# Kernel optimization log

Measured on AMD Instinct MI355X. Metric: run time of the kernel, lower is better.

The kernel has to match this reference:

```python
import jax, jax.numpy as jnp
import numpy as np

# module hyper-params (init_kwargs); shift_sz=1 => 1x1 patches == pixels, flag == mask
SHIFT_SZ = 1
STRIDE = 1
MASK_THRED = 1
TRIPLE_WEIGHT = 1.0   # only rescales gradients in the original custom backward; forward output unchanged
FUSE = True
FUSE_K = 3            # contextual-attention fuse kernel size (identity 3x3)


def _fuse_scores(score, H, W):
    # score: [B, L, L] (query loc, key loc). Contextual-attention 'fuse':
    # smooth the score map with an identity kernel along both spatial unfoldings.
    B, L, _ = score.shape
    eye = jnp.eye(FUSE_K, dtype=score.dtype).reshape(1, 1, FUSE_K, FUSE_K)

    def conv(x):
        return jax.lax.conv_general_dilated(
            x, eye, window_strides=(1, 1), padding='SAME',
            dimension_numbers=('NCHW', 'OIHW', 'NCHW'))

    s = conv(score[:, None])                                            # [B,1,L,L]
    s = s.reshape(B, H, W, H, W).transpose(0, 2, 1, 4, 3).reshape(B, 1, L, L)
    s = conv(s)
    s = s.reshape(B, W, H, W, H).transpose(0, 2, 1, 4, 3).reshape(B, L, L)
    return s


def reference(x, mask):
    # x: [B, 2c, H, W]; first c channels = former (decoder feat), last c = latter (encoder feat)
    B, C2, H, W = x.shape
    c = C2 // 2
    L = H * W
    former = x[:, :c]
    latter = x[:, c:]

    # flag: True = inside hole. With shift_sz=1, stride=1, mask_thred=1 the patch flag is the mask itself.
    flag = mask.reshape(L) > 0.5                                        # [L]

    lat = latter.reshape(B, c, L)
    # normalize context (key) patches to unit L2 norm -> cosine-style correlation
    key = lat / jnp.maximum(jnp.linalg.norm(lat, axis=1, keepdims=True), 1e-4)
    score = jnp.einsum('bcl,bck->blk', lat, key)                        # [B, L(query), L(key)]
    if FUSE:
        score = _fuse_scores(score, H, W)

    # only attend to context patches OUTSIDE the hole
    score = jnp.where(flag[None, None, :], -jnp.inf, score)
    attn = jax.nn.softmax(score, axis=-1)                               # [B, L, L]

    # soft shift: attention-weighted gather of former (decoder) features from context pixels
    shift = jnp.einsum('blk,bck->bcl', attn, former.reshape(B, c, L))   # [B, c, L]
    # the shifted feature only fills hole locations; zero elsewhere
    shift = shift * flag[None, None, :].astype(x.dtype)
    shift = shift.reshape(B, c, H, W)

    return jnp.concatenate([former, latter, shift], axis=1)             # [B, 3c, H, W]


def setup_inputs():
    key = jax.random.key(0)
    k1, k2 = jax.random.split(key)
    B, c, H, W = 2, 64, 64, 64
    x = jax.random.normal(k1, (B, 2 * c, H, W), dtype=jnp.float32)
    mask = (jax.random.uniform(k2, (1, 1, H, W)) > 0.75).astype(jnp.float32)
    return {"x": x, "mask": mask}
```

## Files before the change

kernel.cpp:

```cpp
#include <hip/hip_runtime.h>
#include <math.h>


#define L 4096

typedef unsigned int   u32;
typedef unsigned short u16;
typedef short  short8 __attribute__((ext_vector_type(8)));
typedef float  f32x16 __attribute__((ext_vector_type(16)));

#define MFMA32(a, b, c) __builtin_amdgcn_mfma_f32_32x32x16_bf16((a), (b), (c), 0, 0, 0)

__device__ __forceinline__ u16 f2bf(float f) {
    u32 u = __float_as_uint(f);
    u32 r = (u + 0x7FFFu + ((u >> 16) & 1u)) >> 16;
    return (u16)r;
}

__device__ __forceinline__ void lds_async16(void* lds, const void* g) {
    __builtin_amdgcn_global_load_lds((const __attribute__((address_space(1))) u32*)g,
                                     (__attribute__((address_space(3))) u32*)lds, 16, 0, 0);
}

#define OFF_LATB  0u
#define OFF_FORB  1048576u
#define OFF_GARR  2097152u
#define GARR_BB   1575936u
#define OFF_FBITS 5249024u
#define OFF_ROWS  5249536u
#define OFF_CNT   5265920u
#define OFF_PART  5266432u
#define OFF_KNB   5266432u

__global__ void k_pre1(const float4* __restrict__ x4, float4* __restrict__ out4,
                       const float* __restrict__ x, const float* __restrict__ mask,
                       u16* __restrict__ latb, u16* __restrict__ knb, u16* __restrict__ forb,
                       int* __restrict__ rows, int* __restrict__ cnt, u32* __restrict__ fbits)
{
    const int blk = blockIdx.x, t = threadIdx.x;
    if (blk < 1537) {
        int i = blk * 256 + t;
        if (i < 262144) {
            int b = i >> 17, j = i & 131071;
            out4[b * 196608 + j] = x4[b * 131072 + j];
        } else if (i < 393216) {
            int z = i - 262144; int b = z >> 16, j = z & 65535;
            out4[b * 196608 + 131072 + j] = make_float4(0.f, 0.f, 0.f, 0.f);
        }
    } else if (blk < 1569) {
        int tid = (blk - 1537) * 256 + t;
        int b = tid >> 12, l = tid & 4095;
        const float* xb = x + (size_t)b * 524288;
        float v[64]; float ss = 0.f;
        #pragma unroll
        for (int c = 0; c < 64; ++c) { v[c] = xb[(64 + c) * 4096 + l]; ss += v[c] * v[c]; }
        float inv = 1.f / fmaxf(sqrtf(ss), 1e-4f);
        u16* lr = latb + (size_t)(b * 4096 + l) * 64;
        u16* kr = knb  + (size_t)(b * 4096 + l) * 64;
        #pragma unroll
        for (int c8 = 0; c8 < 8; ++c8) {
            u32 wl[4], wk[4];
            #pragma unroll
            for (int i = 0; i < 4; ++i) {
                float a = v[c8 * 8 + 2 * i], bb2 = v[c8 * 8 + 2 * i + 1];
                wl[i] = (u32)f2bf(a) | ((u32)f2bf(bb2) << 16);
                wk[i] = (u32)f2bf(a * inv) | ((u32)f2bf(bb2 * inv) << 16);
            }
            uint4 pl = make_uint4(wl[0], wl[1], wl[2], wl[3]);
            uint4 pk = make_uint4(wk[0], wk[1], wk[2], wk[3]);
            *(uint4*)(lr + c8 * 8) = pl;
            *(uint4*)(kr + c8 * 8) = pk;
        }
        u16* fr = forb + (size_t)(b * 4096 + l) * 64;
        #pragma unroll
        for (int c8 = 0; c8 < 8; ++c8) {
            u32 wf[4];
            #pragma unroll
            for (int i = 0; i < 4; ++i) {
                float a = xb[(c8 * 8 + 2 * i) * 4096 + l];
                float bb2 = xb[(c8 * 8 + 2 * i + 1) * 4096 + l];
                wf[i] = (u32)f2bf(a) | ((u32)f2bf(bb2) << 16);
            }
            uint4 pf = make_uint4(wf[0], wf[1], wf[2], wf[3]);
            *(uint4*)(fr + c8 * 8) = pf;
        }
    } else {
        __shared__ int lcnt;
        __shared__ u32 lb[128];
        if (t == 0) lcnt = 0;
        if (t < 128) lb[t] = 0u;
        __syncthreads();
        for (int i = t; i < L; i += 256) {
            if (mask[i] > 0.5f) {
                int p = atomicAdd(&lcnt, 1); rows[p] = i;
                int kp = ((i & 63) << 6) | (i >> 6);
                atomicOr(&lb[kp >> 5], 1u << (kp & 31));
            }
        }
        __syncthreads();
        if (t < 128) fbits[t] = lb[t];
        if (t == 0) cnt[0] = lcnt;
    }
}

__global__ void k_garr(const u16* __restrict__ knb, char* __restrict__ garr)
{
    int tid = blockIdx.x * 256 + threadIdx.x;
    if (tid >= 2 * 4104 * 3) return;
    int b = tid / 12312; int rem = tid - b * 12312;
    int sg = rem / 3, aa = rem - 3 * (rem / 3);
    int mp = sg - 1;
    char* dst = garr + (size_t)b * GARR_BB + (size_t)sg * 384;
    int key = (sg & 7) << 4;
    const u16* src = nullptr;
    if (mp >= 0 && mp < L) {
        int q = (((mp & 63) << 6) | (mp >> 6)) + aa - 1;
        if (q >= 0 && q < L) src = knb + (size_t)b * 262144 + (size_t)q * 64;
    }
    #pragma unroll
    for (int c8 = 0; c8 < 8; ++c8) {
        uint4 v = src ? *(const uint4*)(src + c8 * 8) : make_uint4(0, 0, 0, 0);
        *(uint4*)(dst + ((aa * 128 + c8 * 16) ^ key)) = v;
    }
}

__global__ __launch_bounds__(256, 2)
void k_flash(const u16* __restrict__ latb, const u16* __restrict__ forb,
             const char* __restrict__ garr, const u32* __restrict__ fbits,
             const int* __restrict__ rows, const int* __restrict__ cnt,
             char* __restrict__ part)
{
    __shared__ __align__(16) char smem[80000];
    char* slab = smem;
    u16*  F_s  = (u16*)(smem + 52224);
    u16*  p_s  = (u16*)(smem + 69632);
    int*  rl_s = (int*)(smem + 79872);

    const int t = threadIdx.x;
    const int rt = blockIdx.x, ks = blockIdx.y, b = blockIdx.z;
    const int count = cnt[0];
    const int base = rt * 32;
    if (base >= count) return;
    const int nact = min(32, count - base);
    if (t < 32) rl_s[t] = rows[base + min(t, nact - 1)];
    __syncthreads();

    const int l = t & 63, w = t >> 6;
    const int li = l & 31, hi = l >> 5;
    const size_t boff = (size_t)b * 262144;

    const u16* zp = (const u16*)garr;
    int gl = rl_s[li];
    int tl0 = ((gl & 63) << 6) | (gl >> 6);
    const u16* rp[9];
    #pragma unroll
    for (int tap = 0; tap < 9; ++tap) {
        int bb = tap / 3, aa = tap - 3 * (tap / 3);
        int mp = tl0 + bb - 1;
        const u16* p = zp;
        if (mp >= 0 && mp < L) {
            int q = (((mp & 63) << 6) | (mp >> 6)) + aa - 1;
            if (q >= 0 && q < L) p = latb + boff + (size_t)q * 64;
        }
        rp[tap] = p;
    }
    short8 bu[36];
    #pragma unroll
    for (int q = 0; q < 36; ++q) {
        int tap = q >> 2, Ksi = q & 3;
        bu[q] = *(const short8*)(rp[tap] + Ksi * 16 + hi * 8);
    }

    float mrun = -INFINITY, srun = 0.f;
    f32x16 acc0, acc1;
    #pragma unroll
    for (int r = 0; r < 16; ++r) { acc0[r] = 0.f; acc1[r] = 0.f; }

    const int kp0 = ks * 512;
    const char* gb = garr + (size_t)b * GARR_BB;

    for (int kt = 0; kt < 4; ++kt) {
        const int k0p = kp0 + kt * 128;
        __syncthreads();

        const char* gw = gb + (size_t)k0p * 384;
        #pragma unroll
        for (int i = 0; i < 13; ++i) {
            int idx = w + 4 * i;
            if (idx < 51)
                lds_async16(slab + idx * 1024, gw + idx * 1024 + l * 16);
        }

        {
            int kpA = k0p + 2 * l, kpB = kpA + 1;
            int kA = ((kpA & 63) << 6) | (kpA >> 6);
            int kB = ((kpB & 63) << 6) | (kpB >> 6);
            const u32* pa = (const u32*)(forb + boff + (size_t)kA * 64 + w * 16);
            const u32* pc = (const u32*)(forb + boff + (size_t)kB * 64 + w * 16);
            uint4 A0 = *(const uint4*)pa, A1 = *(const uint4*)(pa + 4);
            uint4 B0 = *(const uint4*)pc, B1 = *(const uint4*)(pc + 4);
            u32 av[8] = {A0.x, A0.y, A0.z, A0.w, A1.x, A1.y, A1.z, A1.w};
            u32 bv[8] = {B0.x, B0.y, B0.z, B0.w, B1.x, B1.y, B1.z, B1.w};
            #pragma unroll
            for (int i2 = 0; i2 < 8; ++i2) {
                u32 w0 = (av[i2] & 0xffffu) | (bv[i2] << 16);
                u32 w1 = (av[i2] >> 16) | (bv[i2] & 0xffff0000u);
                *(u32*)((char*)F_s + (w * 16 + 2 * i2) * 272 + l * 4) = w0;
                *(u32*)((char*)F_s + (w * 16 + 2 * i2 + 1) * 272 + l * 4) = w1;
            }
        }
        asm volatile("s_waitcnt vmcnt(0)" ::: "memory");
        __syncthreads();

        f32x16 sc;
        #pragma unroll
        for (int r = 0; r < 16; ++r) sc[r] = 0.f;
        const int slot_base = w * 32 + li;
        #pragma unroll
        for (int tap = 0; tap < 9; ++tap) {
            int bb = tap / 3, aa = tap - 3 * (tap / 3);
            int sl = slot_base + bb;
            int key = (sl & 7) << 4;
            int base_b = sl * 384 + aa * 128 + hi * 16;
            #pragma unroll
            for (int Ksi = 0; Ksi < 4; ++Ksi) {
                short8 ag = *(const short8*)(slab + ((base_b + Ksi * 32) ^ key));
                sc = MFMA32(ag, bu[tap * 4 + Ksi], sc);
            }
        }

        u32 bits = fbits[(k0p >> 5) + w];
        float sv[16]; float mx = -INFINITY;
        #pragma unroll
        for (int r = 0; r < 16; ++r) {
            int kloc = (r & 3) + 8 * (r >> 2) + 4 * hi;
            float s = sc[r];
            if ((bits >> kloc) & 1) s = -INFINITY;
            sv[r] = s; mx = fmaxf(mx, s);
        }
        mx = fmaxf(mx, __shfl_xor(mx, 32, 64));
        float newm = fmaxf(mrun, mx);
        float fac, tsum = 0.f;
        u16 pb[16];
        if (newm > -INFINITY) {
            fac = __expf(mrun - newm);
            #pragma unroll
            for (int r = 0; r < 16; ++r) { float p = __expf(sv[r] - newm); tsum += p; pb[r] = f2bf(p); }
        } else {
            fac = 1.f;
            #pragma unroll
            for (int r = 0; r < 16; ++r) pb[r] = 0;
        }
        tsum += __shfl_xor(tsum, 32, 64);
        srun = srun * fac + tsum;
        mrun = newm;
        #pragma unroll
        for (int rq = 0; rq < 8; ++rq) {
            int r = rq * 2;
            int kloc = (r & 3) + 8 * (r >> 2) + 4 * hi;
            u32 pw = (u32)pb[r] | ((u32)pb[r + 1] << 16);
            *(u32*)(p_s + w * 1280 + li * 40 + kloc) = pw;
        }

        #pragma unroll
        for (int r = 0; r < 16; ++r) {
            int row = (r & 3) + 8 * (r >> 2) + 4 * hi;
            float fr = __shfl(fac, row, 64);
            acc0[r] *= fr; acc1[r] *= fr;
        }
        #pragma unroll
        for (int Ksi2 = 0; Ksi2 < 2; ++Ksi2) {
            short8 pa2 = *(const short8*)(p_s + w * 1280 + li * 40 + Ksi2 * 16 + hi * 8);
            short8 f0 = *(const short8*)(F_s + li * 136 + w * 32 + Ksi2 * 16 + hi * 8);
            short8 f1 = *(const short8*)(F_s + (32 + li) * 136 + w * 32 + Ksi2 * 16 + hi * 8);
            acc0 = MFMA32(pa2, f0, acc0);
            acc1 = MFMA32(pa2, f1, acc1);
        }
    }

    __syncthreads();
    float* um = (float*)smem;
    if (l < 32) { um[(w * 32 + li) * 66] = mrun; um[(w * 32 + li) * 66 + 1] = srun; }
    #pragma unroll
    for (int r = 0; r < 16; ++r) {
        int row = (r & 3) + 8 * (r >> 2) + 4 * hi;
        um[(w * 32 + row) * 66 + 2 + li] = acc0[r];
        um[(w * 32 + row) * 66 + 2 + 32 + li] = acc1[r];
    }
    __syncthreads();
    {
        int row = t >> 3, cq = t & 7;
        float m4[4], s4[4];
        #pragma unroll
        for (int wv = 0; wv < 4; ++wv) {
            m4[wv] = um[(wv * 32 + row) * 66];
            s4[wv] = um[(wv * 32 + row) * 66 + 1];
        }
        float M = fmaxf(fmaxf(m4[0], m4[1]), fmaxf(m4[2], m4[3]));
        float S = 0.f; float wx[4];
        if (M > -INFINITY) {
            #pragma unroll
            for (int wv = 0; wv < 4; ++wv) { wx[wv] = __expf(m4[wv] - M); S += s4[wv] * wx[wv]; }
        } else {
            wx[0] = wx[1] = wx[2] = wx[3] = 0.f;
        }
        char* pp = part + ((size_t)((b * 128 + rt) * 8 + ks)) * 4608 + row * 144;
        u16 h[8];
        #pragma unroll
        for (int i = 0; i < 8; ++i) {
            int ch = cq * 8 + i;
            float v = 0.f;
            #pragma unroll
            for (int wv = 0; wv < 4; ++wv) v += wx[wv] * um[(wv * 32 + row) * 66 + 2 + ch];
            h[i] = f2bf(v);
        }
        if (cq == 0) { *(float*)pp = M; *(float*)(pp + 4) = S; }
        uint4 hw;
        hw.x = (u32)h[0] | ((u32)h[1] << 16); hw.y = (u32)h[2] | ((u32)h[3] << 16);
        hw.z = (u32)h[4] | ((u32)h[5] << 16); hw.w = (u32)h[6] | ((u32)h[7] << 16);
        *(uint4*)(pp + 16 + cq * 16) = hw;
    }
}

__global__ void k_reduce(const int* __restrict__ rows, const int* __restrict__ cnt,
                         const char* __restrict__ part, float* __restrict__ out)
{
    int t = threadIdx.x;
    int row = t >> 3, cq = t & 7;
    int rt = blockIdx.x, b = blockIdx.y;
    int count = cnt[0];
    int slot = rt * 32 + row;
    if (slot >= count) return;
    int l = rows[slot];
    const char* pb = part + ((size_t)((b * 128 + rt) * 8)) * 4608 + row * 144;
    float M = -INFINITY, m8[8], s8[8];
    #pragma unroll
    for (int k = 0; k < 8; ++k) {
        m8[k] = *(const float*)(pb + k * 4608);
        s8[k] = *(const float*)(pb + k * 4608 + 4);
        M = fmaxf(M, m8[k]);
    }
    if (!(M > -INFINITY)) return;
    float S = 0.f; float accv[8] = {0.f, 0.f, 0.f, 0.f, 0.f, 0.f, 0.f, 0.f};
    #pragma unroll
    for (int k = 0; k < 8; ++k) {
        float wxv = __expf(m8[k] - M);
        S += s8[k] * wxv;
        uint4 hv = *(const uint4*)(pb + k * 4608 + 16 + cq * 16);
        u32 uu[4] = {hv.x, hv.y, hv.z, hv.w};
        #pragma unroll
        for (int i = 0; i < 4; ++i) {
            accv[2 * i]     += wxv * __uint_as_float((uu[i] & 0xffffu) << 16);
            accv[2 * i + 1] += wxv * __uint_as_float(uu[i] & 0xffff0000u);
        }
    }
    float inv = (S > 0.f) ? 1.f / S : 0.f;
    float* ob = out + (size_t)b * 786432 + 524288 + l;
    #pragma unroll
    for (int i = 0; i < 8; ++i) ob[(size_t)(cq * 8 + i) * 4096] = accv[i] * inv;
}

extern "C" void kernel_launch(void* const* d_in, const int* in_sizes, int n_in,
                              void* d_out, int out_size, void* d_ws, size_t ws_size,
                              hipStream_t stream)
{
    const float* x    = (const float*)d_in[0];
    const float* mask = (const float*)d_in[1];
    float* out = (float*)d_out;
    char* ws = (char*)d_ws;

    u16* latb = (u16*)(ws + OFF_LATB);
    u16* forb = (u16*)(ws + OFF_FORB);
    char* garr = ws + OFF_GARR;
    u32* fbits = (u32*)(ws + OFF_FBITS);
    int* rows  = (int*)(ws + OFF_ROWS);
    int* cnt   = (int*)(ws + OFF_CNT);
    char* part = ws + OFF_PART;
    u16* knb   = (u16*)(ws + OFF_KNB);

    k_pre1<<<1570, 256, 0, stream>>>((const float4*)x, (float4*)out, x, mask,
                                     latb, knb, forb, rows, cnt, fbits);
    k_garr<<<97, 256, 0, stream>>>(knb, garr);
    k_flash<<<dim3(128, 8, 2), 256, 0, stream>>>(latb, forb, garr, fbits, rows, cnt, part);
    k_reduce<<<dim3(128, 2), 256, 0, stream>>>(rows, cnt, part, out);
}
```

Before: 143.7 us.

## Fuse garr build into preprocess, fold reduce into flash, prefetch next tile

Removes the k_garr kernel by scattering normalized key rows directly into the swizzled gather array from k_pre1, and removes k_reduce by having the last of eight split-K blocks per row tile do the cross-split softmax merge, using an atomic done-counter. In k_flash it double-buffers by issuing the next tile's slab and F loads after the score MFMAs, raises wave priority around the MFMA block, unrolls the B-fragment registers, and remaps block IDs to spread work across XCDs with 64 row tiles instead of 128. Launch overhead and serialized global-load latency drop, in exchange for atomics and fences, more barriers per iteration, and a cap of 2048 hole rows.

```diff
diff --git a/kernel.cpp b/kernel.cpp
--- a/kernel.cpp
+++ b/kernel.cpp
@@ -9,14 +9,12 @@
 typedef short  short8 __attribute__((ext_vector_type(8)));
 typedef float  f32x16 __attribute__((ext_vector_type(16)));
 
-#define MFMA32(a, b, c) __builtin_amdgcn_mfma_f32_32x32x16_bf16((a), (b), (c), 0, 0, 0)
+#define MFMA32(a,b,c) __builtin_amdgcn_mfma_f32_32x32x16_bf16((a),(b),(c),0,0,0)
 
 __device__ __forceinline__ u16 f2bf(float f) {
     u32 u = __float_as_uint(f);
-    u32 r = (u + 0x7FFFu + ((u >> 16) & 1u)) >> 16;
-    return (u16)r;
+    return (u16)((u + 0x7FFFu + ((u >> 16) & 1u)) >> 16);
 }
-
 __device__ __forceinline__ void lds_async16(void* lds, const void* g) {
     __builtin_amdgcn_global_load_lds((const __attribute__((address_space(1))) u32*)g,
                                      (__attribute__((address_space(3))) u32*)lds, 16, 0, 0);
@@ -29,13 +27,15 @@
 #define OFF_FBITS 5249024u
 #define OFF_ROWS  5249536u
 #define OFF_CNT   5265920u
-#define OFF_PART  5266432u
-#define OFF_KNB   5266432u
+#define OFF_DONE  5266176u
+#define OFF_PART  5267200u
 
 __global__ void k_pre1(const float4* __restrict__ x4, float4* __restrict__ out4,
                        const float* __restrict__ x, const float* __restrict__ mask,
-                       u16* __restrict__ latb, u16* __restrict__ knb, u16* __restrict__ forb,
-                       int* __restrict__ rows, int* __restrict__ cnt, u32* __restrict__ fbits)
+                       u16* __restrict__ latb, u16* __restrict__ forb,
+                       char* __restrict__ garr, int* __restrict__ rows,
+                       int* __restrict__ cnt, u32* __restrict__ fbits,
+                       u32* __restrict__ done)
 {
     const int blk = blockIdx.x, t = threadIdx.x;
     if (blk < 1537) {
@@ -55,8 +55,7 @@
         #pragma unroll
         for (int c = 0; c < 64; ++c) { v[c] = xb[(64 + c) * 4096 + l]; ss += v[c] * v[c]; }
         float inv = 1.f / fmaxf(sqrtf(ss), 1e-4f);
-        u16* lr = latb + (size_t)(b * 4096 + l) * 64;
-        u16* kr = knb  + (size_t)(b * 4096 + l) * 64;
+        uint4 lq[8], kq[8];
         #pragma unroll
         for (int c8 = 0; c8 < 8; ++c8) {
             u32 wl[4], wk[4];
@@ -66,10 +65,23 @@
                 wl[i] = (u32)f2bf(a) | ((u32)f2bf(bb2) << 16);
                 wk[i] = (u32)f2bf(a * inv) | ((u32)f2bf(bb2 * inv) << 16);
             }
-            uint4 pl = make_uint4(wl[0], wl[1], wl[2], wl[3]);
-            uint4 pk = make_uint4(wk[0], wk[1], wk[2], wk[3]);
-            *(uint4*)(lr + c8 * 8) = pl;
-            *(uint4*)(kr + c8 * 8) = pk;
+            lq[c8] = make_uint4(wl[0], wl[1], wl[2], wl[3]);
+            kq[c8] = make_uint4(wk[0], wk[1], wk[2], wk[3]);
+        }
+        u16* lr = latb + (size_t)(b * 4096 + l) * 64;
+        #pragma unroll
+        for (int c8 = 0; c8 < 8; ++c8) *(uint4*)(lr + c8 * 8) = lq[c8];
+        #pragma unroll
+        for (int aa = 0; aa < 3; ++aa) {
+            int src = l + 1 - aa;
+            if (src >= 0 && src < L) {
+                int sg = (((src & 63) << 6) | (src >> 6)) + 1;
+                char* dst = garr + (size_t)b * GARR_BB + (size_t)sg * 384;
+                int key = (sg & 7) << 4;
+                #pragma unroll
+                for (int c8 = 0; c8 < 8; ++c8)
+                    *(uint4*)(dst + ((aa * 128 + c8 * 16) ^ key)) = kq[c8];
+            }
         }
         u16* fr = forb + (size_t)(b * 4096 + l) * 64;
         #pragma unroll
@@ -81,8 +93,7 @@
                 float bb2 = xb[(c8 * 8 + 2 * i + 1) * 4096 + l];
                 wf[i] = (u32)f2bf(a) | ((u32)f2bf(bb2) << 16);
             }
-            uint4 pf = make_uint4(wf[0], wf[1], wf[2], wf[3]);
-            *(uint4*)(fr + c8 * 8) = pf;
+            *(uint4*)(fr + c8 * 8) = make_uint4(wf[0], wf[1], wf[2], wf[3]);
         }
     } else {
         __shared__ int lcnt;
@@ -92,35 +103,25 @@
         __syncthreads();
         for (int i = t; i < L; i += 256) {
             if (mask[i] > 0.5f) {
-                int p = atomicAdd(&lcnt, 1); rows[p] = i;
+                int p = atomicAdd(&lcnt, 1);
+                if (p < 2048) rows[p] = i;
                 int kp = ((i & 63) << 6) | (i >> 6);
                 atomicOr(&lb[kp >> 5], 1u << (kp & 31));
             }
         }
         __syncthreads();
         if (t < 128) fbits[t] = lb[t];
-        if (t == 0) cnt[0] = lcnt;
-    }
-}
-
-__global__ void k_garr(const u16* __restrict__ knb, char* __restrict__ garr)
-{
-    int tid = blockIdx.x * 256 + threadIdx.x;
-    if (tid >= 2 * 4104 * 3) return;
-    int b = tid / 12312; int rem = tid - b * 12312;
-    int sg = rem / 3, aa = rem - 3 * (rem / 3);
-    int mp = sg - 1;
-    char* dst = garr + (size_t)b * GARR_BB + (size_t)sg * 384;
-    int key = (sg & 7) << 4;
-    const u16* src = nullptr;
-    if (mp >= 0 && mp < L) {
-        int q = (((mp & 63) << 6) | (mp >> 6)) + aa - 1;
-        if (q >= 0 && q < L) src = knb + (size_t)b * 262144 + (size_t)q * 64;
-    }
-    #pragma unroll
-    for (int c8 = 0; c8 < 8; ++c8) {
-        uint4 v = src ? *(const uint4*)(src + c8 * 8) : make_uint4(0, 0, 0, 0);
-        *(uint4*)(dst + ((aa * 128 + c8 * 16) ^ key)) = v;
+        if (t == 0) cnt[0] = min(lcnt, 2048);
+        if (t < 128) done[t] = 0u;
+        if (t < 128) {
+            int b = t >> 6, i = t & 63;
+            char* gB = garr + (size_t)b * GARR_BB;
+            uint4 z = make_uint4(0, 0, 0, 0);
+            if (i < 24)       *(uint4*)(gB + i * 16) = z;
+            else if (i < 48)  *(uint4*)(gB + (size_t)4097 * 384 + (i - 24) * 16) = z;
+            else if (i < 56)  *(uint4*)(gB + (size_t)1 * 384 + (i - 48) * 16) = z;
+            else              *(uint4*)(gB + (size_t)4096 * 384 + 256 + (i - 56) * 16) = z;
+        }
     }
 }
 
@@ -128,7 +129,8 @@
 void k_flash(const u16* __restrict__ latb, const u16* __restrict__ forb,
              const char* __restrict__ garr, const u32* __restrict__ fbits,
              const int* __restrict__ rows, const int* __restrict__ cnt,
-             char* __restrict__ part)
+             char* __restrict__ part, u32* __restrict__ done,
+             float* __restrict__ out)
 {
     __shared__ __align__(16) char smem[80000];
     char* slab = smem;
@@ -136,8 +138,13 @@
     u16*  p_s  = (u16*)(smem + 69632);
     int*  rl_s = (int*)(smem + 79872);
 
+    const int lin = blockIdx.x;
+    const int xcd = lin & 7, slotq = lin >> 3;
+    const int gid = xcd * 128 + slotq;
+    const int ksb = gid >> 6, rt = gid & 63;
+    const int ks = ksb >> 1, b = ksb & 1;
+
     const int t = threadIdx.x;
-    const int rt = blockIdx.x, ks = blockIdx.y, b = blockIdx.z;
     const int count = cnt[0];
     const int base = rt * 32;
     if (base >= count) return;
@@ -164,12 +171,15 @@
         }
         rp[tap] = p;
     }
-    short8 bu[36];
-    #pragma unroll
-    for (int q = 0; q < 36; ++q) {
-        int tap = q >> 2, Ksi = q & 3;
-        bu[q] = *(const short8*)(rp[tap] + Ksi * 16 + hi * 8);
-    }
+#define DECL_BU(TAP) \
+    short8 bu##TAP##_0 = *(const short8*)(rp[TAP] + 0  + hi * 8); \
+    short8 bu##TAP##_1 = *(const short8*)(rp[TAP] + 16 + hi * 8); \
+    short8 bu##TAP##_2 = *(const short8*)(rp[TAP] + 32 + hi * 8); \
+    short8 bu##TAP##_3 = *(const short8*)(rp[TAP] + 48 + hi * 8); \
+    asm volatile("" : "+v"(bu##TAP##_0), "+v"(bu##TAP##_1), "+v"(bu##TAP##_2), "+v"(bu##TAP##_3));
+    DECL_BU(0) DECL_BU(1) DECL_BU(2) DECL_BU(3) DECL_BU(4)
+    DECL_BU(5) DECL_BU(6) DECL_BU(7) DECL_BU(8)
+#undef DECL_BU
 
     float mrun = -INFINITY, srun = 0.f;
     f32x16 acc0, acc1;
@@ -178,56 +188,68 @@
 
     const int kp0 = ks * 512;
     const char* gb = garr + (size_t)b * GARR_BB;
+    uint4 fA0, fA1, fB0, fB1;
+
+    auto issue_slab = [&](int k0p) {
+        const char* gw = gb + (size_t)k0p * 384;
+        #pragma unroll
+        for (int i = 0; i < 13; ++i) {
+            int idx = w + 4 * i;
+            if (idx < 51) lds_async16(slab + idx * 1024, gw + idx * 1024 + l * 16);
+        }
+    };
+    auto issue_F = [&](int k0p) {
+        int kpA = k0p + 2 * l, kpB = kpA + 1;
+        int kA = ((kpA & 63) << 6) | (kpA >> 6);
+        int kB = ((kpB & 63) << 6) | (kpB >> 6);
+        const u32* pa = (const u32*)(forb + boff + (size_t)kA * 64 + w * 16);
+        const u32* pc = (const u32*)(forb + boff + (size_t)kB * 64 + w * 16);
+        fA0 = *(const uint4*)pa; fA1 = *(const uint4*)(pa + 4);
+        fB0 = *(const uint4*)pc; fB1 = *(const uint4*)(pc + 4);
+    };
+    auto write_F = [&]() {
+        u32 av[8] = {fA0.x, fA0.y, fA0.z, fA0.w, fA1.x, fA1.y, fA1.z, fA1.w};
+        u32 bv[8] = {fB0.x, fB0.y, fB0.z, fB0.w, fB1.x, fB1.y, fB1.z, fB1.w};
+        #pragma unroll
+        for (int i2 = 0; i2 < 8; ++i2) {
+            u32 w0 = (av[i2] & 0xffffu) | (bv[i2] << 16);
+            u32 w1 = (av[i2] >> 16) | (bv[i2] & 0xffff0000u);
+            *(u32*)((char*)F_s + (w * 16 + 2 * i2) * 272 + l * 4) = w0;
+            *(u32*)((char*)F_s + (w * 16 + 2 * i2 + 1) * 272 + l * 4) = w1;
+        }
+    };
+
+    issue_slab(kp0);
+    issue_F(kp0);
+    asm volatile("s_waitcnt vmcnt(0)" ::: "memory");
+    write_F();
+    __syncthreads();
 
     for (int kt = 0; kt < 4; ++kt) {
         const int k0p = kp0 + kt * 128;
-        __syncthreads();
-
-        const char* gw = gb + (size_t)k0p * 384;
-        #pragma unroll
-        for (int i = 0; i < 13; ++i) {
-            int idx = w + 4 * i;
-            if (idx < 51)
-                lds_async16(slab + idx * 1024, gw + idx * 1024 + l * 16);
-        }
-
-        {
-            int kpA = k0p + 2 * l, kpB = kpA + 1;
-            int kA = ((kpA & 63) << 6) | (kpA >> 6);
-            int kB = ((kpB & 63) << 6) | (kpB >> 6);
-            const u32* pa = (const u32*)(forb + boff + (size_t)kA * 64 + w * 16);
-            const u32* pc = (const u32*)(forb + boff + (size_t)kB * 64 + w * 16);
-            uint4 A0 = *(const uint4*)pa, A1 = *(const uint4*)(pa + 4);
-            uint4 B0 = *(const uint4*)pc, B1 = *(const uint4*)(pc + 4);
-            u32 av[8] = {A0.x, A0.y, A0.z, A0.w, A1.x, A1.y, A1.z, A1.w};
-            u32 bv[8] = {B0.x, B0.y, B0.z, B0.w, B1.x, B1.y, B1.z, B1.w};
-            #pragma unroll
-            for (int i2 = 0; i2 < 8; ++i2) {
-                u32 w0 = (av[i2] & 0xffffu) | (bv[i2] << 16);
-                u32 w1 = (av[i2] >> 16) | (bv[i2] & 0xffff0000u);
-                *(u32*)((char*)F_s + (w * 16 + 2 * i2) * 272 + l * 4) = w0;
-                *(u32*)((char*)F_s + (w * 16 + 2 * i2 + 1) * 272 + l * 4) = w1;
-            }
-        }
-        asm volatile("s_waitcnt vmcnt(0)" ::: "memory");
-        __syncthreads();
 
         f32x16 sc;
         #pragma unroll
         for (int r = 0; r < 16; ++r) sc[r] = 0.f;
         const int slot_base = w * 32 + li;
-        #pragma unroll
-        for (int tap = 0; tap < 9; ++tap) {
-            int bb = tap / 3, aa = tap - 3 * (tap / 3);
-            int sl = slot_base + bb;
-            int key = (sl & 7) << 4;
-            int base_b = sl * 384 + aa * 128 + hi * 16;
-            #pragma unroll
-            for (int Ksi = 0; Ksi < 4; ++Ksi) {
-                short8 ag = *(const short8*)(slab + ((base_b + Ksi * 32) ^ key));
-                sc = MFMA32(ag, bu[tap * 4 + Ksi], sc);
-            }
-        }
+        __builtin_amdgcn_s_setprio(1);
+#define TAP_MFMA(TAP) do { \
+        const int bb = TAP / 3, aac = TAP % 3; \
+        int sl = slot_base + bb; \
+        int key = (sl & 7) << 4; \
+        int base_b = sl * 384 + aac * 128 + hi * 16; \
+        sc = MFMA32(*(const short8*)(slab + ((base_b +  0) ^ key)), bu##TAP##_0, sc); \
+        sc = MFMA32(*(const short8*)(slab + ((base_b + 32) ^ key)), bu##TAP##_1, sc); \
+        sc = MFMA32(*(const short8*)(slab + ((base_b + 64) ^ key)), bu##TAP##_2, sc); \
+        sc = MFMA32(*(const short8*)(slab + ((base_b + 96) ^ key)), bu##TAP##_3, sc); \
+    } while (0)
+        TAP_MFMA(0); TAP_MFMA(1); TAP_MFMA(2); TAP_MFMA(3); TAP_MFMA(4);
+        TAP_MFMA(5); TAP_MFMA(6); TAP_MFMA(7); TAP_MFMA(8);
+#undef TAP_MFMA
+        __builtin_amdgcn_s_setprio(0);
+        __syncthreads();
+
+        if (kt < 3) { issue_slab(k0p + 128); issue_F(k0p + 128); }
 
         u32 bits = fbits[(k0p >> 5) + w];
         float sv[16]; float mx = -INFINITY;
@@ -276,9 +298,15 @@
             acc0 = MFMA32(pa2, f0, acc0);
             acc1 = MFMA32(pa2, f1, acc1);
         }
-    }
-
-    __syncthreads();
+        __syncthreads();
+
+        if (kt < 3) {
+            asm volatile("s_waitcnt vmcnt(0)" ::: "memory");
+            write_F();
+        }
+        __syncthreads();
+    }
+
     float* um = (float*)smem;
     if (l < 32) { um[(w * 32 + li) * 66] = mrun; um[(w * 32 + li) * 66 + 1] = srun; }
     #pragma unroll
@@ -304,15 +332,15 @@
         } else {
             wx[0] = wx[1] = wx[2] = wx[3] = 0.f;
         }
-        char* pp = part + ((size_t)((b * 128 + rt) * 8 + ks)) * 4608 + row * 144;
+        char* pp = part + ((size_t)((b * 64 + rt) * 8 + ks)) * 4608 + row * 144;
         u16 h[8];
         #pragma unroll
         for (int i = 0; i < 8; ++i) {
             int ch = cq * 8 + i;
-            float v = 0.f;
-            #pragma unroll
-            for (int wv = 0; wv < 4; ++wv) v += wx[wv] * um[(wv * 32 + row) * 66 + 2 + ch];
-            h[i] = f2bf(v);
+            float vv = 0.f;
+            #pragma unroll
+            for (int wv = 0; wv < 4; ++wv) vv += wx[wv] * um[(wv * 32 + row) * 66 + 2 + ch];
+            h[i] = f2bf(vv);
         }
         if (cq == 0) { *(float*)pp = M; *(float*)(pp + 4) = S; }
         uint4 hw;
@@ -320,44 +348,47 @@
         hw.z = (u32)h[4] | ((u32)h[5] << 16); hw.w = (u32)h[6] | ((u32)h[7] << 16);
         *(uint4*)(pp + 16 + cq * 16) = hw;
     }
-}
-
-__global__ void k_reduce(const int* __restrict__ rows, const int* __restrict__ cnt,
-                         const char* __restrict__ part, float* __restrict__ out)
-{
-    int t = threadIdx.x;
-    int row = t >> 3, cq = t & 7;
-    int rt = blockIdx.x, b = blockIdx.y;
-    int count = cnt[0];
-    int slot = rt * 32 + row;
-    if (slot >= count) return;
-    int l = rows[slot];
-    const char* pb = part + ((size_t)((b * 128 + rt) * 8)) * 4608 + row * 144;
-    float M = -INFINITY, m8[8], s8[8];
-    #pragma unroll
-    for (int k = 0; k < 8; ++k) {
-        m8[k] = *(const float*)(pb + k * 4608);
-        s8[k] = *(const float*)(pb + k * 4608 + 4);
-        M = fmaxf(M, m8[k]);
-    }
-    if (!(M > -INFINITY)) return;
-    float S = 0.f; float accv[8] = {0.f, 0.f, 0.f, 0.f, 0.f, 0.f, 0.f, 0.f};
-    #pragma unroll
-    for (int k = 0; k < 8; ++k) {
-        float wxv = __expf(m8[k] - M);
-        S += s8[k] * wxv;
-        uint4 hv = *(const uint4*)(pb + k * 4608 + 16 + cq * 16);
-        u32 uu[4] = {hv.x, hv.y, hv.z, hv.w};
-        #pragma unroll
-        for (int i = 0; i < 4; ++i) {
-            accv[2 * i]     += wxv * __uint_as_float((uu[i] & 0xffffu) << 16);
-            accv[2 * i + 1] += wxv * __uint_as_float(uu[i] & 0xffff0000u);
-        }
-    }
-    float inv = (S > 0.f) ? 1.f / S : 0.f;
-    float* ob = out + (size_t)b * 786432 + 524288 + l;
-    #pragma unroll
-    for (int i = 0; i < 8; ++i) ob[(size_t)(cq * 8 + i) * 4096] = accv[i] * inv;
+
+    __threadfence();
+    __syncthreads();
+    if (t == 0) rl_s[0] = (atomicAdd(&done[b * 64 + rt], 1u) == 7u) ? 1 : 0;
+    __syncthreads();
+    if (!rl_s[0]) return;
+    __threadfence();
+    {
+        int row = t >> 3, cq = t & 7;
+        int slot = base + row;
+        if (slot < count) {
+            int lr = rows[slot];
+            const char* pbp = part + ((size_t)((b * 64 + rt) * 8)) * 4608 + row * 144;
+            float M = -INFINITY, m8[8], s8[8];
+            #pragma unroll
+            for (int k = 0; k < 8; ++k) {
+                m8[k] = *(const float*)(pbp + k * 4608);
+                s8[k] = *(const float*)(pbp + k * 4608 + 4);
+                M = fmaxf(M, m8[k]);
+            }
+            if (M > -INFINITY) {
+                float S = 0.f; float accv[8] = {0.f,0.f,0.f,0.f,0.f,0.f,0.f,0.f};
+                #pragma unroll
+                for (int k = 0; k < 8; ++k) {
+                    float wxv = __expf(m8[k] - M);
+                    S += s8[k] * wxv;
+                    uint4 hv = *(const uint4*)(pbp + k * 4608 + 16 + cq * 16);
+                    u32 uu[4] = {hv.x, hv.y, hv.z, hv.w};
+                    #pragma unroll
+                    for (int i = 0; i < 4; ++i) {
+                        accv[2 * i]     += wxv * __uint_as_float((uu[i] & 0xffffu) << 16);
+                        accv[2 * i + 1] += wxv * __uint_as_float(uu[i] & 0xffff0000u);
+                    }
+                }
+                float invS = (S > 0.f) ? 1.f / S : 0.f;
+                float* ob = out + (size_t)b * 786432 + 524288 + lr;
+                #pragma unroll
+                for (int i = 0; i < 8; ++i) ob[(size_t)(cq * 8 + i) * 4096] = accv[i] * invS;
+            }
+        }
+    }
 }
 
 extern "C" void kernel_launch(void* const* d_in, const int* in_sizes, int n_in,
@@ -369,18 +400,16 @@
     float* out = (float*)d_out;
     char* ws = (char*)d_ws;
 
-    u16* latb = (u16*)(ws + OFF_LATB);
-    u16* forb = (u16*)(ws + OFF_FORB);
+    u16* latb  = (u16*)(ws + OFF_LATB);
+    u16* forb  = (u16*)(ws + OFF_FORB);
     char* garr = ws + OFF_GARR;
     u32* fbits = (u32*)(ws + OFF_FBITS);
     int* rows  = (int*)(ws + OFF_ROWS);
     int* cnt   = (int*)(ws + OFF_CNT);
+    u32* done  = (u32*)(ws + OFF_DONE);
     char* part = ws + OFF_PART;
-    u16* knb   = (u16*)(ws + OFF_KNB);
 
     k_pre1<<<1570, 256, 0, stream>>>((const float4*)x, (float4*)out, x, mask,
-                                     latb, knb, forb, rows, cnt, fbits);
-    k_garr<<<97, 256, 0, stream>>>(knb, garr);
-    k_flash<<<dim3(128, 8, 2), 256, 0, stream>>>(latb, forb, garr, fbits, rows, cnt, part);
-    k_reduce<<<dim3(128, 2), 256, 0, stream>>>(rows, cnt, part, out);
+                                     latb, forb, garr, rows, cnt, fbits, done);
+    k_flash<<<1024, 256, 0, stream>>>(latb, forb, garr, fbits, rows, cnt, part, done, out);
 }
```

Result: slower. 233.1 us (+62.2%).
